# Kernel tuning notes

Measured on AMD Instinct MI355X. Metric: run time of the kernel, lower is better.

## Reference

```python
import jax, jax.numpy as jnp
import numpy as np

ETYPES = ((0, 2), (4, 6))  # per-metapath edge-type indices into the doubled r_vec table
ALPHA = 3.0


def celu3(x):
    return jax.nn.celu(x, alpha=ALPHA)


def cmul(a, b):
    # complex multiply, last dim = (real, imag)
    re = a[..., 0] * b[..., 0] - a[..., 1] * b[..., 1]
    im = a[..., 0] * b[..., 1] + a[..., 1] * b[..., 0]
    return jnp.stack([re, im], axis=-1)


def setup_inputs() -> dict:
    key = jax.random.key(0)
    ks = jax.random.split(key, 10)
    N, H, heads, M, E, P = 50000, 64, 4, 2, 250000, 3
    R, FH = 4, 128
    D = heads * H
    return {
        "features": jax.random.normal(ks[0], (N, H), jnp.float32),
        "r_vec": jax.random.normal(ks[1], (R, H // 2, 2), jnp.float32),
        "attn1_w": jax.random.normal(ks[2], (heads, H), jnp.float32) * 0.1,
        "attn2": jax.random.normal(ks[3], (1, heads, H), jnp.float32) * 0.1,
        "fw1": jax.random.normal(ks[4], (2 * FH, D), jnp.float32) * 0.05,
        "fb1": jnp.zeros((2 * FH,), jnp.float32),
        "fw2": jax.random.normal(ks[5], (FH, 2 * FH), jnp.float32) * 0.05,
        "fb2": jnp.zeros((FH,), jnp.float32),
        "fw3": jax.random.normal(ks[6], (1, FH), jnp.float32) * 0.05,
        "instances": jax.random.randint(ks[7], (M, E, P), 0, N, jnp.int32),
    }


def reference(features, r_vec, attn1_w, attn2, fw1, fb1, fw2, fb2, fw3, instances):
    N, H = features.shape
    M, E, P = instances.shape
    heads = attn1_w.shape[0]
    # unit-modulus rotations + conjugates: [2R, H/2, 2], even=r, odd=conj(r)
    rv = r_vec / jnp.linalg.norm(r_vec, axis=2, keepdims=True)
    conj = rv * jnp.array([1.0, -1.0], rv.dtype)
    rv2 = jnp.stack([rv, conj], axis=1).reshape(-1, H // 2, 2)

    per_path = []
    for m in range(M):
        inst = instances[m]  # [E, P]
        # backward cumulative rotation: final_r[i] = prod_{j>=i} r_{etype[j]}, final_r[P-1]=1
        ident = jnp.stack([jnp.ones(H // 2, rv.dtype), jnp.zeros(H // 2, rv.dtype)], axis=-1)
        frs = [ident]
        for i in range(P - 2, -1, -1):
            frs.insert(0, cmul(frs[0], rv2[ETYPES[m][i]]))
        fr = jnp.stack(frs)  # [P, H/2, 2]
        # gather features along metapath and rotate (last position rotated by identity)
        edata = features[inst].reshape(E, P, H // 2, 2)
        rot = cmul(edata, fr[None])
        me = jnp.mean(rot.reshape(E, P, H), axis=1)  # [E, H]
        se = celu3(me) * jax.nn.sigmoid(me)  # gated metapath embedding
        eft = celu3(se)  # same across heads in original (tiled)
        seg = inst[:, 0]  # target node per instance
        a1 = celu3(features[seg] @ attn1_w.T)  # [E, heads]
        a2 = jnp.einsum('eh,kh->ek', eft, attn2[0])  # [E, heads]
        a = celu3(a1 + a2)
        # segment softmax over each node's instance set
        amax = jax.ops.segment_max(a, seg, num_segments=N)
        ex = jnp.exp(a - amax[seg])
        den = jax.ops.segment_sum(ex, seg, num_segments=N)
        attn = ex / den[seg]  # [E, heads]
        hsum = jax.ops.segment_sum(attn[:, :, None] * eft[:, None, :], seg, num_segments=N)
        per_path.append(celu3(hsum).reshape(N, heads * H))  # empty nodes -> 0

    z = jnp.stack(per_path, axis=1)  # [N, M, D]
    t = celu3(z @ fw1.T + fb1)
    t = celu3(t @ fw2.T + fb2)
    w = (t @ fw3.T).mean(axis=0)  # [M, 1]
    beta = jax.nn.softmax(w, axis=0)
    out = (beta * z).sum(axis=1)  # [N, D]
    return out
```

## Files before the change

kernel.cpp:

```cpp
#include <hip/hip_runtime.h>
#include <hip/hip_bf16.h>

typedef unsigned short u16;
typedef unsigned int   u32;
typedef short bf16x8 __attribute__((ext_vector_type(8)));
typedef float f32x4  __attribute__((ext_vector_type(4)));

#define CAP 64

__device__ inline float b2f(u16 u){ return __builtin_bit_cast(float, (u32)u << 16); }
__device__ inline u16 f2b(float f){
  u32 x = __builtin_bit_cast(u32, f);
  x += 0x7fffu + ((x >> 16) & 1u);
  return (u16)(x >> 16);
}
__device__ inline u32 pk2(float lo, float hi){
  float2 f; f.x = lo; f.y = hi;
  __hip_bfloat162 h = __float22bfloat162_rn(f);
  u32 r; __builtin_memcpy(&r, &h, 4);
  return r;
}
__device__ inline void up2(u32 u, float& lo, float& hi){
  lo = __builtin_bit_cast(float, u << 16);
  hi = __builtin_bit_cast(float, u & 0xffff0000u);
}
__device__ inline float fexp(float x){ return __expf(x); }
__device__ inline float frcp(float x){ return __builtin_amdgcn_rcpf(x); }
__device__ inline float celu3(float x){
  return x > 0.f ? x : 3.f * (__expf(x * (1.f/3.f)) - 1.f);
}
__device__ inline float act1(float x){
  float u  = __expf(x * (1.f/3.f));
  float u3 = u*u*u;
  float sg = u3 * frcp(u3 + 1.f);
  float c1 = x > 0.f ? x : 3.f*u - 3.f;
  float se = c1 * sg;
  return se > 0.f ? se : se + se*se*(1.f/6.f);
}

__global__ __launch_bounds__(256) void pre_kernel(
    const float* __restrict__ feat, const float* __restrict__ attn1,
    const float* __restrict__ rvec, const float* __restrict__ fw1,
    const float* __restrict__ fw2,
    u16* __restrict__ featb, u16* __restrict__ rotA, u16* __restrict__ rotB,
    float* __restrict__ a1c, u16* __restrict__ fw1b, u16* __restrict__ fw2b,
    int* __restrict__ cnt, float* __restrict__ wacc,
    int N, int nbA)
{
  __shared__ float w1s[256], rvs[256];
  int b = blockIdx.x, t = threadIdx.x;
  if (b >= nbA){
    int cb = b - nbA;
    if (cb < 48){
      const float* src = (cb < 32) ? fw1 : fw2;
      u16* dst = (cb < 32) ? fw1b : fw2b;
      int i = (cb < 32 ? cb : cb - 32)*256 + t;
      float4 a = ((const float4*)src)[2*i], bb = ((const float4*)src)[2*i + 1];
      uint4 o;
      o.x = pk2(a.x, a.y);  o.y = pk2(a.z, a.w);
      o.z = pk2(bb.x, bb.y); o.w = pk2(bb.z, bb.w);
      ((uint4*)dst)[i] = o;
      return;
    }
    cb -= 48;
    int i = cb*256 + t;
    if (i*4 < 2*N) ((uint4*)cnt)[i] = make_uint4(0u,0u,0u,0u);
    if (cb == 0 && t < 128) wacc[t] = 0.f;
    return;
  }
  w1s[t] = attn1[t];
  rvs[t] = rvec[t];
  __syncthreads();
  int g = t >> 4, l = t & 15;
  int n = b * 16 + g;
  if (n >= N) return;
  float4 x = ((const float4*)feat)[(size_t)n*16 + l];
  float4 xs;
  xs.x = x.x*(1.f/3.f); xs.y = x.y*(1.f/3.f);
  xs.z = x.z*(1.f/3.f); xs.w = x.w*(1.f/3.f);
  uint2 o;
  o.x = pk2(xs.x, xs.y);
  o.y = pk2(xs.z, xs.w);
  ((uint2*)featb)[(size_t)n*16 + l] = o;

  #pragma unroll
  for (int m = 0; m < 2; ++m){
    float4 ra = *(const float4*)&rvs[(2*m)*64 + l*4];
    float4 rb = *(const float4*)&rvs[(2*m+1)*64 + l*4];
    float na0 = rsqrtf(ra.x*ra.x + ra.y*ra.y); ra.x*=na0; ra.y*=na0;
    float na1 = rsqrtf(ra.z*ra.z + ra.w*ra.w); ra.z*=na1; ra.w*=na1;
    float nb0 = rsqrtf(rb.x*rb.x + rb.y*rb.y); rb.x*=nb0; rb.y*=nb0;
    float nb1 = rsqrtf(rb.z*rb.z + rb.w*rb.w); rb.z*=nb1; rb.w*=nb1;
    float A0r = rb.x*ra.x - rb.y*ra.y, A0i = rb.x*ra.y + rb.y*ra.x;
    float A1r = rb.z*ra.z - rb.w*ra.w, A1i = rb.z*ra.w + rb.w*ra.z;
    uint2 oa, ob;
    oa.x = pk2(xs.x*A0r - xs.y*A0i, xs.x*A0i + xs.y*A0r);
    oa.y = pk2(xs.z*A1r - xs.w*A1i, xs.z*A1i + xs.w*A1r);
    ob.x = pk2(xs.x*rb.x - xs.y*rb.y, xs.x*rb.y + xs.y*rb.x);
    ob.y = pk2(xs.z*rb.z - xs.w*rb.w, xs.z*rb.w + xs.w*rb.z);
    ((uint2*)rotA)[((size_t)m*N + n)*16 + l] = oa;
    ((uint2*)rotB)[((size_t)m*N + n)*16 + l] = ob;
  }

  float d[4];
  #pragma unroll
  for (int k = 0; k < 4; ++k){
    int wb = k*64 + l*4;
    d[k] = x.x*w1s[wb] + x.y*w1s[wb+1] + x.z*w1s[wb+2] + x.w*w1s[wb+3];
  }
  #pragma unroll
  for (int off = 8; off; off >>= 1){
    #pragma unroll
    for (int k = 0; k < 4; ++k) d[k] += __shfl_xor(d[k], off);
  }
  if (l == 0){
    float4 av;
    av.x = celu3(d[0]); av.y = celu3(d[1]);
    av.z = celu3(d[2]); av.w = celu3(d[3]);
    ((float4*)a1c)[n] = av;
  }
}

__global__ __launch_bounds__(256) void edge_kernel(
    const u16* __restrict__ rotA, const u16* __restrict__ rotB,
    const u16* __restrict__ featb, const int* __restrict__ inst,
    const float* __restrict__ a1c, const float* __restrict__ attn2,
    u16* __restrict__ eft, float* __restrict__ a_ws,
    int* __restrict__ cnt, int* __restrict__ bucket, int E, int N)
{
  __shared__ float w2s[256];
  int m = blockIdx.y;
  int t = threadIdx.x;
  w2s[t] = attn2[t];
  __syncthreads();

  int g = t >> 3, l = t & 7;
  int e0 = blockIdx.x * 64 + g;
  int e1 = e0 + 32;
  bool ok0 = e0 < E, ok1 = e1 < E;
  int ec0 = ok0 ? e0 : 0, ec1 = ok1 ? e1 : 0;
  size_t mN = (size_t)m * N;
  size_t mE = (size_t)m * E;

  int b0 = (int)((mE + ec0)*3), b1 = (int)((mE + ec1)*3);
  int i00 = inst[b0], i01 = inst[b0+1], i02 = inst[b0+2];
  int i10 = inst[b1], i11 = inst[b1+1], i12 = inst[b1+2];

  uint4 v00 = ((const uint4*)rotA)[(mN + i00)*8 + l];
  uint4 v01 = ((const uint4*)rotB)[(mN + i01)*8 + l];
  uint4 v02 = ((const uint4*)featb)[(size_t)i02*8 + l];
  uint4 v10 = ((const uint4*)rotA)[(mN + i10)*8 + l];
  uint4 v11 = ((const uint4*)rotB)[(mN + i11)*8 + l];
  uint4 v12 = ((const uint4*)featb)[(size_t)i12*8 + l];

  float A[8], B[8], C[8], ef0[8], ef1[8];
  up2(v00.x, A[0], A[1]); up2(v00.y, A[2], A[3]);
  up2(v00.z, A[4], A[5]); up2(v00.w, A[6], A[7]);
  up2(v01.x, B[0], B[1]); up2(v01.y, B[2], B[3]);
  up2(v01.z, B[4], B[5]); up2(v01.w, B[6], B[7]);
  up2(v02.x, C[0], C[1]); up2(v02.y, C[2], C[3]);
  up2(v02.z, C[4], C[5]); up2(v02.w, C[6], C[7]);
  #pragma unroll
  for (int c = 0; c < 8; ++c) ef0[c] = act1(A[c] + B[c] + C[c]);

  up2(v10.x, A[0], A[1]); up2(v10.y, A[2], A[3]);
  up2(v10.z, A[4], A[5]); up2(v10.w, A[6], A[7]);
  up2(v11.x, B[0], B[1]); up2(v11.y, B[2], B[3]);
  up2(v11.z, B[4], B[5]); up2(v11.w, B[6], B[7]);
  up2(v12.x, C[0], C[1]); up2(v12.y, C[2], C[3]);
  up2(v12.z, C[4], C[5]); up2(v12.w, C[6], C[7]);
  #pragma unroll
  for (int c = 0; c < 8; ++c) ef1[c] = act1(A[c] + B[c] + C[c]);

  if (ok0){
    uint4 uo;
    uo.x = pk2(ef0[0], ef0[1]); uo.y = pk2(ef0[2], ef0[3]);
    uo.z = pk2(ef0[4], ef0[5]); uo.w = pk2(ef0[6], ef0[7]);
    ((uint4*)eft)[(mE + e0)*8 + l] = uo;
  }
  if (ok1){
    uint4 uo;
    uo.x = pk2(ef1[0], ef1[1]); uo.y = pk2(ef1[2], ef1[3]);
    uo.z = pk2(ef1[4], ef1[5]); uo.w = pk2(ef1[6], ef1[7]);
    ((uint4*)eft)[(mE + e1)*8 + l] = uo;
  }

  float d20[4], d21[4];
  #pragma unroll
  for (int k = 0; k < 4; ++k){
    int wb = k*64 + l*8;
    float4 wA = *(const float4*)&w2s[wb];
    float4 wB = *(const float4*)&w2s[wb+4];
    d20[k] = ef0[0]*wA.x + ef0[1]*wA.y + ef0[2]*wA.z + ef0[3]*wA.w
           + ef0[4]*wB.x + ef0[5]*wB.y + ef0[6]*wB.z + ef0[7]*wB.w;
    d21[k] = ef1[0]*wA.x + ef1[1]*wA.y + ef1[2]*wA.z + ef1[3]*wA.w
           + ef1[4]*wB.x + ef1[5]*wB.y + ef1[6]*wB.z + ef1[7]*wB.w;
  }
  #pragma unroll
  for (int off = 4; off; off >>= 1){
    #pragma unroll
    for (int k = 0; k < 4; ++k){
      d20[k] += __shfl_xor(d20[k], off);
      d21[k] += __shfl_xor(d21[k], off);
    }
  }
  if (l == 0){
    if (ok0){
      float4 a1v4 = ((const float4*)a1c)[i00];
      float4 av;
      av.x = celu3(a1v4.x + d20[0]);
      av.y = celu3(a1v4.y + d20[1]);
      av.z = celu3(a1v4.z + d20[2]);
      av.w = celu3(a1v4.w + d20[3]);
      ((float4*)a_ws)[mE + e0] = av;
      int pos = atomicAdd(&cnt[m*N + i00], 1);
      if (pos < CAP) bucket[(size_t)(m*N + i00)*CAP + pos] = e0;
    }
    if (ok1){
      float4 a1v4 = ((const float4*)a1c)[i10];
      float4 av;
      av.x = celu3(a1v4.x + d21[0]);
      av.y = celu3(a1v4.y + d21[1]);
      av.z = celu3(a1v4.z + d21[2]);
      av.w = celu3(a1v4.w + d21[3]);
      ((float4*)a_ws)[mE + e1] = av;
      int pos = atomicAdd(&cnt[m*N + i10], 1);
      if (pos < CAP) bucket[(size_t)(m*N + i10)*CAP + pos] = e1;
    }
  }
}

__global__ __launch_bounds__(256) void seg_kernel(
    const float* __restrict__ a_ws, const u16* __restrict__ eft,
    const int* __restrict__ cnt, const int* __restrict__ bucket,
    u16* __restrict__ z, int E, int N)
{
  __shared__ float wls[8][64][4];
  __shared__ int   els[8][64];
  int tid = threadIdx.x;
  int wvb = tid >> 6;
  int lane = tid & 63;
  int half = lane >> 5, l = lane & 31;
  int seg = wvb*2 + half;
  int m = blockIdx.y;
  int n = blockIdx.x * 8 + seg;
  bool valid = n < N;
  int sidx = m*N + (valid ? n : 0);
  int deg = 0;
  if (valid){ deg = cnt[sidx]; deg = deg > CAP ? CAP : deg; }
  size_t ebase = (size_t)m * E;
  const int* bk = bucket + (size_t)sidx * CAP;

  float w0a=0.f,w1a=0.f,w2a=0.f,w3a=0.f, w0b=0.f,w1b=0.f,w2b=0.f,w3b=0.f;
  int ea = 0, eb = 0;
  if (l < deg){
    ea = bk[l];
    float4 av = ((const float4*)a_ws)[ebase + ea];
    w0a=fexp(av.x); w1a=fexp(av.y); w2a=fexp(av.z); w3a=fexp(av.w);
  }
  if (l + 32 < deg){
    eb = bk[l+32];
    float4 av = ((const float4*)a_ws)[ebase + eb];
    w0b=fexp(av.x); w1b=fexp(av.y); w2b=fexp(av.z); w3b=fexp(av.w);
  }
  els[seg][l]    = ea;
  els[seg][l+32] = eb;
  *(float4*)&wls[seg][l][0]    = make_float4(w0a,w1a,w2a,w3a);
  *(float4*)&wls[seg][l+32][0] = make_float4(w0b,w1b,w2b,w3b);

  float d0=w0a+w0b, d1=w1a+w1b, d2=w2a+w2b, d3=w3a+w3b;
  #pragma unroll
  for (int off = 16; off; off >>= 1){
    d0 += __shfl_xor(d0, off); d1 += __shfl_xor(d1, off);
    d2 += __shfl_xor(d2, off); d3 += __shfl_xor(d3, off);
  }

  float hA0=0.f,hA1=0.f,hA2=0.f,hA3=0.f;
  float hB0=0.f,hB1=0.f,hB2=0.f,hB3=0.f;
  const u32* ep = (const u32*)eft;
  int j = 0;
  for (; j + 1 < deg; j += 2){
    int ej0 = els[seg][j], ej1 = els[seg][j+1];
    u32 p0 = ep[(ebase + ej0)*32 + l];
    u32 p1 = ep[(ebase + ej1)*32 + l];
    float4 wj0 = *(const float4*)&wls[seg][j][0];
    float4 wj1 = *(const float4*)&wls[seg][j+1][0];
    float eva, evb;
    up2(p0, eva, evb);
    hA0 += wj0.x*eva; hA1 += wj0.y*eva; hA2 += wj0.z*eva; hA3 += wj0.w*eva;
    hB0 += wj0.x*evb; hB1 += wj0.y*evb; hB2 += wj0.z*evb; hB3 += wj0.w*evb;
    up2(p1, eva, evb);
    hA0 += wj1.x*eva; hA1 += wj1.y*eva; hA2 += wj1.z*eva; hA3 += wj1.w*eva;
    hB0 += wj1.x*evb; hB1 += wj1.y*evb; hB2 += wj1.z*evb; hB3 += wj1.w*evb;
  }
  if (j < deg){
    int ej0 = els[seg][j];
    u32 p0 = ep[(ebase + ej0)*32 + l];
    float4 wj0 = *(const float4*)&wls[seg][j][0];
    float eva, evb;
    up2(p0, eva, evb);
    hA0 += wj0.x*eva; hA1 += wj0.y*eva; hA2 += wj0.z*eva; hA3 += wj0.w*eva;
    hB0 += wj0.x*evb; hB1 += wj0.y*evb; hB2 += wj0.z*evb; hB3 += wj0.w*evb;
  }
  float r0 = deg > 0 ? frcp(d0) : 0.f;
  float r1 = deg > 0 ? frcp(d1) : 0.f;
  float r2 = deg > 0 ? frcp(d2) : 0.f;
  float r3 = deg > 0 ? frcp(d3) : 0.f;
  if (valid){
    u32* zr = (u32*)(z + (size_t)sidx*256) + l;
    zr[0]  = pk2(celu3(hA0*r0), celu3(hB0*r0));
    zr[32] = pk2(celu3(hA1*r1), celu3(hB1*r1));
    zr[64] = pk2(celu3(hA2*r2), celu3(hB2*r2));
    zr[96] = pk2(celu3(hA3*r3), celu3(hB3*r3));
  }
}

__global__ __launch_bounds__(512, 2) void mlp_kernel(
    const u16* __restrict__ z, const u16* __restrict__ fw1b, const float* __restrict__ fb1,
    const u16* __restrict__ fw2b, const float* __restrict__ fb2, const float* __restrict__ fw3,
    float* __restrict__ waccP, int rows, int N)
{
  __shared__ u16 buf[64][264];
  __shared__ float fw3s[128];
  __shared__ float sPart[8][64];
  int tid = threadIdx.x;
  int wv = tid >> 6, lane = tid & 63, lr = lane & 15, quad = lane >> 4;
  f32x4 zero4 = {0.f, 0.f, 0.f, 0.f};

  const u16* wb1 = fw1b + (size_t)(wv*32 + lr)*256 + quad*8;
  bf16x8 B1[2][8];
  #pragma unroll
  for (int nt = 0; nt < 2; ++nt)
    #pragma unroll
    for (int ks = 0; ks < 8; ++ks)
      B1[nt][ks] = *(const bf16x8*)(wb1 + nt*16*256 + ks*32);
  #pragma unroll
  for (int nt = 0; nt < 2; ++nt)
    #pragma unroll
    for (int ks = 0; ks < 8; ++ks)
      asm volatile("" :: "v"(B1[nt][ks]));

  const u16* wb2 = fw2b + (size_t)(wv*16 + lr)*256 + quad*8;
  if (tid < 128) fw3s[tid] = fw3[tid];

  const uint4* zg = (const uint4*)z;
  int ntiles = (rows + 63) >> 6;
  int gstride = gridDim.x;
  int tile = blockIdx.x;

  uint4 zr4[4];
  {
    int row0 = tile * 64;
    #pragma unroll
    for (int it = 0; it < 4; ++it){
      int idx = it*512 + tid;
      int row = idx >> 5, c8 = idx & 31;
      int gr = row0 + row;
      zr4[it] = make_uint4(0u,0u,0u,0u);
      if (gr < rows) zr4[it] = zg[(size_t)gr*32 + c8];
    }
  }

  for (; tile < ntiles; ){
    int row0 = tile * 64;
    #pragma unroll
    for (int it = 0; it < 4; ++it){
      int idx = it*512 + tid;
      int row = idx >> 5, c8 = idx & 31;
      *(uint4*)&buf[row][c8*8] = zr4[it];
    }
    __syncthreads();

    int tnext = tile + gstride;
    uint4 zn[4];
    {
      int nrow0 = tnext * 64;
      #pragma unroll
      for (int it = 0; it < 4; ++it){
        int idx = it*512 + tid;
        int row = idx >> 5, c8 = idx & 31;
        int gr = nrow0 + row;
        zn[it] = make_uint4(0u,0u,0u,0u);
        if (tnext < ntiles && gr < rows) zn[it] = zg[(size_t)gr*32 + c8];
      }
    }

    f32x4 acc[4][2];
    #pragma unroll
    for (int a = 0; a < 4; ++a){ acc[a][0] = zero4; acc[a][1] = zero4; }
    #pragma unroll
    for (int ks = 0; ks < 8; ++ks){
      #pragma unroll
      for (int mt = 0; mt < 4; ++mt){
        bf16x8 af = *(const bf16x8*)&buf[mt*16 + lr][ks*32 + quad*8];
        acc[mt][0] = __builtin_amdgcn_mfma_f32_16x16x32_bf16(af, B1[0][ks], acc[mt][0], 0, 0, 0);
        acc[mt][1] = __builtin_amdgcn_mfma_f32_16x16x32_bf16(af, B1[1][ks], acc[mt][1], 0, 0, 0);
      }
    }

    bf16x8 B2[8];
    #pragma unroll
    for (int ks = 0; ks < 8; ++ks)
      B2[ks] = *(const bf16x8*)(wb2 + ks*32);

    __syncthreads();
    #pragma unroll
    for (int nt = 0; nt < 2; ++nt){
      int col = wv*32 + nt*16 + lr;
      float bias = fb1[col];
      #pragma unroll
      for (int mt = 0; mt < 4; ++mt)
        #pragma unroll
        for (int ri = 0; ri < 4; ++ri){
          int row = mt*16 + quad*4 + ri;
          buf[row][col] = f2b(celu3(acc[mt][nt][ri] + bias));
        }
    }
    __syncthreads();

    f32x4 acc2[4];
    #pragma unroll
    for (int a = 0; a < 4; ++a) acc2[a] = zero4;
    #pragma unroll
    for (int ks = 0; ks < 8; ++ks){
      #pragma unroll
      for (int mt = 0; mt < 4; ++mt){
        bf16x8 af = *(const bf16x8*)&buf[mt*16 + lr][ks*32 + quad*8];
        acc2[mt] = __builtin_amdgcn_mfma_f32_16x16x32_bf16(af, B2[ks], acc2[mt], 0, 0, 0);
      }
    }

    {
      int col = wv*16 + lr;
      float bias2 = fb2[col];
      float w3 = fw3s[col];
      float ps[4][4];
      #pragma unroll
      for (int mt = 0; mt < 4; ++mt)
        #pragma unroll
        for (int ri = 0; ri < 4; ++ri)
          ps[mt][ri] = celu3(acc2[mt][ri] + bias2) * w3;
      #pragma unroll
      for (int off = 8; off; off >>= 1)
        #pragma unroll
        for (int mt = 0; mt < 4; ++mt)
          #pragma unroll
          for (int ri = 0; ri < 4; ++ri)
            ps[mt][ri] += __shfl_xor(ps[mt][ri], off);
      if (lr == 0){
        #pragma unroll
        for (int mt = 0; mt < 4; ++mt)
          #pragma unroll
          for (int ri = 0; ri < 4; ++ri)
            sPart[wv][mt*16 + quad*4 + ri] = ps[mt][ri];
      }
    }
    __syncthreads();

    if (tid < 64){
      float s = 0.f;
      #pragma unroll
      for (int w = 0; w < 8; ++w) s += sPart[w][tid];
      int gr = row0 + tid;
      if (gr >= rows) s = 0.f;
      float s0 = (gr < N) ? s : 0.f;
      float s1 = (gr < N) ? 0.f : s;
      #pragma unroll
      for (int off = 32; off; off >>= 1){
        s0 += __shfl_xor(s0, off);
        s1 += __shfl_xor(s1, off);
      }
      if (tid == 0){
        int slot = tile & 63;
        atomicAdd(&waccP[slot],      s0);
        atomicAdd(&waccP[64 + slot], s1);
      }
    }

    #pragma unroll
    for (int it = 0; it < 4; ++it) zr4[it] = zn[it];
    tile = tnext;
  }
}

__global__ __launch_bounds__(256) void out_kernel(
    const u16* __restrict__ z, const float* __restrict__ wacc,
    float* __restrict__ out, int total, float invN)
{
  __shared__ float bsh[2];
  int tid = threadIdx.x;
  if (tid < 64){
    float s0 = wacc[tid], s1 = wacc[64 + tid];
    #pragma unroll
    for (int off = 32; off; off >>= 1){
      s0 += __shfl_xor(s0, off);
      s1 += __shfl_xor(s1, off);
    }
    if (tid == 0){
      float w0 = s0*invN, w1 = s1*invN;
      float mx = fmaxf(w0, w1);
      float e0 = __expf(w0 - mx), e1 = __expf(w1 - mx);
      float s = e0 + e1;
      bsh[0] = e0 / s;
      bsh[1] = e1 / s;
    }
  }
  __syncthreads();
  float b0 = bsh[0], b1 = bsh[1];
  int idx = blockIdx.x * 256 + tid;
  if (idx*8 >= total) return;
  uint4 u0 = ((const uint4*)z)[idx];
  uint4 u1 = ((const uint4*)z)[(total >> 3) + idx];
  float a0,a1v,c0,c1;
  float4 o;
  up2(u0.x, a0, a1v); up2(u1.x, c0, c1);
  o.x = b0*a0 + b1*c0; o.y = b0*a1v + b1*c1;
  up2(u0.y, a0, a1v); up2(u1.y, c0, c1);
  o.z = b0*a0 + b1*c0; o.w = b0*a1v + b1*c1;
  ((float4*)out)[idx*2] = o;
  up2(u0.z, a0, a1v); up2(u1.z, c0, c1);
  o.x = b0*a0 + b1*c0; o.y = b0*a1v + b1*c1;
  up2(u0.w, a0, a1v); up2(u1.w, c0, c1);
  o.z = b0*a0 + b1*c0; o.w = b0*a1v + b1*c1;
  ((float4*)out)[idx*2 + 1] = o;
}

extern "C" void kernel_launch(void* const* d_in, const int* in_sizes, int n_in,
                              void* d_out, int out_size, void* d_ws, size_t ws_size,
                              hipStream_t stream)
{
  (void)n_in; (void)out_size; (void)ws_size;
  const float* feat  = (const float*)d_in[0];
  const float* rvec  = (const float*)d_in[1];
  const float* attn1 = (const float*)d_in[2];
  const float* attn2 = (const float*)d_in[3];
  const float* fw1   = (const float*)d_in[4];
  const float* fb1   = (const float*)d_in[5];
  const float* fw2   = (const float*)d_in[6];
  const float* fb2   = (const float*)d_in[7];
  const float* fw3   = (const float*)d_in[8];
  const int*   inst  = (const int*)d_in[9];

  int N = in_sizes[0] / 64;
  int E = in_sizes[9] / 6;

  char* ws = (char*)d_ws;
  u16*   z      = (u16*)ws;                            size_t zB = (size_t)2*N*256*2;
  u16*   eft    = (u16*)(ws + zB);                     size_t eB = (size_t)2*E*64*2;
  float* a_ws   = (float*)(ws + zB + eB);              size_t aB = (size_t)2*E*4*4;
  int*   bucket = (int*)(ws + zB + eB + aB);           size_t bB = (size_t)2*N*CAP*4;
  int*   cnt    = (int*)(ws + zB + eB + aB + bB);      size_t cB = (size_t)2*N*4;
  u16*   featb  = (u16*)(ws + zB + eB + aB + bB + cB); size_t fB = (size_t)N*64*2;
  float* a1c    = (float*)(ws + zB + eB + aB + bB + cB + fB);  size_t a1B = (size_t)N*4*4;
  u16*   fw1b   = (u16*)(ws + zB + eB + aB + bB + cB + fB + a1B);
  u16*   fw2b   = fw1b + 256*256;
  float* wacc   = (float*)(fw2b + 128*256);

  u16* rotA = z;
  u16* rotB = z + (size_t)2*N*64;

  int nbA = (N + 15)/16;
  int nbZ = ((2*N)/4 + 255)/256;
  pre_kernel<<<nbA + 48 + nbZ, 256, 0, stream>>>(
      feat, attn1, rvec, fw1, fw2, featb, rotA, rotB, a1c, fw1b, fw2b,
      cnt, wacc, N, nbA);
  edge_kernel<<<dim3((E + 63)/64, 2), 256, 0, stream>>>(
      rotA, rotB, featb, inst, a1c, attn2, eft, a_ws, cnt, bucket, E, N);
  seg_kernel<<<dim3((N + 7)/8, 2), 256, 0, stream>>>(a_ws, eft, cnt, bucket, z, E, N);
  mlp_kernel<<<512, 512, 0, stream>>>(z, fw1b, fb1, fw2b, fb2, fw3, wacc, 2*N, N);
  out_kernel<<<((N*256/8) + 255)/256, 256, 0, stream>>>(z, wacc, (float*)d_out, N*256, 1.f/(float)N);
}
```

Before: 249.5 us.

## Use atomic dynamic tile scheduling and split LDS buffers in MLP kernel

The MLP kernel swaps its static grid-stride tile assignment for dynamic claiming through an atomic counter kept in the workspace and zeroed in the pre-kernel. Separate LDS buffers now hold the z tile and the first-layer activations. This drops one barrier per tile and lets the next z tile be staged into LDS while the second GEMM runs. It aims to balance load across blocks and cut sync stalls, at the cost of more LDS per block (which may limit occupancy) and one atomic per tile.

```diff
diff --git a/kernel.cpp b/kernel.cpp
--- a/kernel.cpp
+++ b/kernel.cpp
@@ -65,7 +65,7 @@
     cb -= 48;
     int i = cb*256 + t;
     if (i*4 < 2*N) ((uint4*)cnt)[i] = make_uint4(0u,0u,0u,0u);
-    if (cb == 0 && t < 128) wacc[t] = 0.f;
+    if (cb == 0 && t < 144) wacc[t] = 0.f;
     return;
   }
   w1s[t] = attn1[t];
@@ -318,11 +318,13 @@
 __global__ __launch_bounds__(512, 2) void mlp_kernel(
     const u16* __restrict__ z, const u16* __restrict__ fw1b, const float* __restrict__ fb1,
     const u16* __restrict__ fw2b, const float* __restrict__ fb2, const float* __restrict__ fw3,
-    float* __restrict__ waccP, int rows, int N)
+    float* __restrict__ waccP, int* __restrict__ tctr, int rows, int N)
 {
-  __shared__ u16 buf[64][264];
+  __shared__ u16 zbuf[64][264];
+  __shared__ u16 t1buf[64][264];
   __shared__ float fw3s[128];
   __shared__ float sPart[8][64];
+  __shared__ int sClaim;
   int tid = threadIdx.x;
   int wv = tid >> 6, lane = tid & 63, lr = lane & 15, quad = lane >> 4;
   f32x4 zero4 = {0.f, 0.f, 0.f, 0.f};
@@ -345,12 +347,12 @@
 
   const uint4* zg = (const uint4*)z;
   int ntiles = (rows + 63) >> 6;
-  int gstride = gridDim.x;
-  int tile = blockIdx.x;
+  int tc = blockIdx.x;
+  if (tc >= ntiles) return;
 
   uint4 zr4[4];
   {
-    int row0 = tile * 64;
+    int row0 = tc * 64;
     #pragma unroll
     for (int it = 0; it < 4; ++it){
       int idx = it*512 + tid;
@@ -359,73 +361,93 @@
       zr4[it] = make_uint4(0u,0u,0u,0u);
       if (gr < rows) zr4[it] = zg[(size_t)gr*32 + c8];
     }
-  }
-
-  for (; tile < ntiles; ){
-    int row0 = tile * 64;
     #pragma unroll
     for (int it = 0; it < 4; ++it){
       int idx = it*512 + tid;
       int row = idx >> 5, c8 = idx & 31;
-      *(uint4*)&buf[row][c8*8] = zr4[it];
+      *(uint4*)&zbuf[row][c8*8] = zr4[it];
+    }
+  }
+  if (tid == 0) sClaim = (int)gridDim.x + atomicAdd(tctr, 1);
+  __syncthreads();
+  int tn = sClaim;
+
+  uint4 zn[4];
+  {
+    int row0 = tn * 64;
+    #pragma unroll
+    for (int it = 0; it < 4; ++it){
+      int idx = it*512 + tid;
+      int row = idx >> 5, c8 = idx & 31;
+      int gr = row0 + row;
+      zn[it] = make_uint4(0u,0u,0u,0u);
+      if (tn < ntiles && gr < rows) zn[it] = zg[(size_t)gr*32 + c8];
+    }
+  }
+
+  while (true){
+    int row0 = tc * 64;
+    if (tid == 0) sClaim = (int)gridDim.x + atomicAdd(tctr, 1);
+
+    f32x4 acc[4][2];
+    #pragma unroll
+    for (int a = 0; a < 4; ++a){ acc[a][0] = zero4; acc[a][1] = zero4; }
+    #pragma unroll
+    for (int ks = 0; ks < 8; ++ks){
+      #pragma unroll
+      for (int mt = 0; mt < 4; ++mt){
+        bf16x8 af = *(const bf16x8*)&zbuf[mt*16 + lr][ks*32 + quad*8];
+        acc[mt][0] = __builtin_amdgcn_mfma_f32_16x16x32_bf16(af, B1[0][ks], acc[mt][0], 0, 0, 0);
+        acc[mt][1] = __builtin_amdgcn_mfma_f32_16x16x32_bf16(af, B1[1][ks], acc[mt][1], 0, 0, 0);
+      }
+    }
+
+    bf16x8 B2[8];
+    #pragma unroll
+    for (int ks = 0; ks < 8; ++ks)
+      B2[ks] = *(const bf16x8*)(wb2 + ks*32);
+
+    #pragma unroll
+    for (int nt = 0; nt < 2; ++nt){
+      int col = wv*32 + nt*16 + lr;
+      float bias = fb1[col];
+      #pragma unroll
+      for (int mt = 0; mt < 4; ++mt)
+        #pragma unroll
+        for (int ri = 0; ri < 4; ++ri){
+          int row = mt*16 + quad*4 + ri;
+          t1buf[row][col] = f2b(celu3(acc[mt][nt][ri] + bias));
+        }
     }
     __syncthreads();
-
-    int tnext = tile + gstride;
-    uint4 zn[4];
+    int tn2 = sClaim;
+
+    #pragma unroll
+    for (int it = 0; it < 4; ++it){
+      int idx = it*512 + tid;
+      int row = idx >> 5, c8 = idx & 31;
+      *(uint4*)&zbuf[row][c8*8] = zn[it];
+    }
     {
-      int nrow0 = tnext * 64;
+      int nrow0 = tn2 * 64;
       #pragma unroll
       for (int it = 0; it < 4; ++it){
         int idx = it*512 + tid;
         int row = idx >> 5, c8 = idx & 31;
         int gr = nrow0 + row;
         zn[it] = make_uint4(0u,0u,0u,0u);
-        if (tnext < ntiles && gr < rows) zn[it] = zg[(size_t)gr*32 + c8];
+        if (tn2 < ntiles && gr < rows) zn[it] = zg[(size_t)gr*32 + c8];
       }
     }
 
-    f32x4 acc[4][2];
-    #pragma unroll
-    for (int a = 0; a < 4; ++a){ acc[a][0] = zero4; acc[a][1] = zero4; }
+    f32x4 acc2[4];
+    #pragma unroll
+    for (int a = 0; a < 4; ++a) acc2[a] = zero4;
     #pragma unroll
     for (int ks = 0; ks < 8; ++ks){
       #pragma unroll
       for (int mt = 0; mt < 4; ++mt){
-        bf16x8 af = *(const bf16x8*)&buf[mt*16 + lr][ks*32 + quad*8];
-        acc[mt][0] = __builtin_amdgcn_mfma_f32_16x16x32_bf16(af, B1[0][ks], acc[mt][0], 0, 0, 0);
-        acc[mt][1] = __builtin_amdgcn_mfma_f32_16x16x32_bf16(af, B1[1][ks], acc[mt][1], 0, 0, 0);
-      }
-    }
-
-    bf16x8 B2[8];
-    #pragma unroll
-    for (int ks = 0; ks < 8; ++ks)
-      B2[ks] = *(const bf16x8*)(wb2 + ks*32);
-
-    __syncthreads();
-    #pragma unroll
-    for (int nt = 0; nt < 2; ++nt){
-      int col = wv*32 + nt*16 + lr;
-      float bias = fb1[col];
-      #pragma unroll
-      for (int mt = 0; mt < 4; ++mt)
-        #pragma unroll
-        for (int ri = 0; ri < 4; ++ri){
-          int row = mt*16 + quad*4 + ri;
-          buf[row][col] = f2b(celu3(acc[mt][nt][ri] + bias));
-        }
-    }
-    __syncthreads();
-
-    f32x4 acc2[4];
-    #pragma unroll
-    for (int a = 0; a < 4; ++a) acc2[a] = zero4;
-    #pragma unroll
-    for (int ks = 0; ks < 8; ++ks){
-      #pragma unroll
-      for (int mt = 0; mt < 4; ++mt){
-        bf16x8 af = *(const bf16x8*)&buf[mt*16 + lr][ks*32 + quad*8];
+        bf16x8 af = *(const bf16x8*)&t1buf[mt*16 + lr][ks*32 + quad*8];
         acc2[mt] = __builtin_amdgcn_mfma_f32_16x16x32_bf16(af, B2[ks], acc2[mt], 0, 0, 0);
       }
     }
@@ -471,15 +493,14 @@
         s1 += __shfl_xor(s1, off);
       }
       if (tid == 0){
-        int slot = tile & 63;
+        int slot = tc & 63;
         atomicAdd(&waccP[slot],      s0);
         atomicAdd(&waccP[64 + slot], s1);
       }
     }
 
-    #pragma unroll
-    for (int it = 0; it < 4; ++it) zr4[it] = zn[it];
-    tile = tnext;
+    tc = tn; tn = tn2;
+    if (tc >= ntiles) break;
   }
 }
 
@@ -555,6 +576,7 @@
   u16*   fw1b   = (u16*)(ws + zB + eB + aB + bB + cB + fB + a1B);
   u16*   fw2b   = fw1b + 256*256;
   float* wacc   = (float*)(fw2b + 128*256);
+  int*   tctr   = (int*)(wacc + 140);
 
   u16* rotA = z;
   u16* rotB = z + (size_t)2*N*64;
@@ -567,6 +589,6 @@
   edge_kernel<<<dim3((E + 63)/64, 2), 256, 0, stream>>>(
       rotA, rotB, featb, inst, a1c, attn2, eft, a_ws, cnt, bucket, E, N);
   seg_kernel<<<dim3((N + 7)/8, 2), 256, 0, stream>>>(a_ws, eft, cnt, bucket, z, E, N);
-  mlp_kernel<<<512, 512, 0, stream>>>(z, fw1b, fb1, fw2b, fb2, fw3, wacc, 2*N, N);
+  mlp_kernel<<<512, 512, 0, stream>>>(z, fw1b, fb1, fw2b, fb2, fw3, wacc, tctr, 2*N, N);
   out_kernel<<<((N*256/8) + 255)/256, 256, 0, stream>>>(z, wacc, (float*)d_out, N*256, 1.f/(float)N);
 }
```

Result: no change. 251.0 us (+0.6%).
